# Kernel optimization log

Hardware: AMD Instinct MI355X
Metric: run time of the kernel (lower is better)

The kernel has to match this reference:

```python
import jax, jax.numpy as jnp
import numpy as np

D_MODEL = 1024
N_HEADS = 16
D_K = D_MODEL // N_HEADS
D_FF = 4096
B, S = 2, 2048
EPS = 1e-5
SCALE = 0.02


def setup_inputs() -> dict:
    key = jax.random.key(0)
    ks = jax.random.split(key, 8)
    return {
        "x": jax.random.normal(ks[0], (B, S, D_MODEL), dtype=jnp.float32),
        "ln1_w": jnp.ones((D_MODEL,), jnp.float32),
        "ln1_b": jnp.zeros((D_MODEL,), jnp.float32),
        "Wq": jax.random.normal(ks[1], (D_MODEL, D_MODEL), jnp.float32) * SCALE,
        "bq": jnp.zeros((D_MODEL,), jnp.float32),
        "Wk": jax.random.normal(ks[2], (D_MODEL, D_MODEL), jnp.float32) * SCALE,
        "bk": jnp.zeros((D_MODEL,), jnp.float32),
        "Wv": jax.random.normal(ks[3], (D_MODEL, D_MODEL), jnp.float32) * SCALE,
        "bv": jnp.zeros((D_MODEL,), jnp.float32),
        "Wo": jax.random.normal(ks[4], (D_MODEL, D_MODEL), jnp.float32) * SCALE,
        "bo": jnp.zeros((D_MODEL,), jnp.float32),
        "ln2_w": jnp.ones((D_MODEL,), jnp.float32),
        "ln2_b": jnp.zeros((D_MODEL,), jnp.float32),
        "W1": jax.random.normal(ks[5], (D_MODEL, D_FF), jnp.float32) * SCALE,
        "b1": jnp.zeros((D_FF,), jnp.float32),
        "W2": jax.random.normal(ks[6], (D_FF, D_MODEL), jnp.float32) * SCALE,
        "b2": jnp.zeros((D_MODEL,), jnp.float32),
    }


def _layernorm(x, w, b):
    mu = jnp.mean(x, axis=-1, keepdims=True)
    var = jnp.mean(jnp.square(x - mu), axis=-1, keepdims=True)
    return (x - mu) * jax.lax.rsqrt(var + EPS) * w + b


def reference(x, ln1_w, ln1_b, Wq, bq, Wk, bk, Wv, bv, Wo, bo,
              ln2_w, ln2_b, W1, b1, W2, b2):
    # Pre-norm multi-head self-attention (dropout = identity, eval mode)
    h = _layernorm(x, ln1_w, ln1_b)                      # [B,S,D]
    q = (h @ Wq + bq).reshape(B, S, N_HEADS, D_K)        # [B,S,H,Dk]
    k = (h @ Wk + bk).reshape(B, S, N_HEADS, D_K)
    v = (h @ Wv + bv).reshape(B, S, N_HEADS, D_K)
    scores = jnp.einsum('bqhd,bkhd->bhqk', q, k) / jnp.sqrt(jnp.float32(D_K))
    attn = jax.nn.softmax(scores, axis=-1)               # [B,H,S,S]
    ctx = jnp.einsum('bhqk,bkhd->bqhd', attn, v).reshape(B, S, D_MODEL)
    x = x + (ctx @ Wo + bo)
    # Pre-norm FFN
    h2 = _layernorm(x, ln2_w, ln2_b)
    ff = jax.nn.relu(h2 @ W1 + b1) @ W2 + b2
    return x + ff
```

## Files before the change

### kernel.cpp

```cpp
#include <hip/hip_runtime.h>
#include <hip/hip_bf16.h>
#include <cstdint>
#include <cstddef>

typedef unsigned short ushort_t;
typedef __bf16 bf16x8 __attribute__((ext_vector_type(8)));
typedef float f32x4 __attribute__((ext_vector_type(4)));
typedef float f32x16 __attribute__((ext_vector_type(16)));

#define D_MODEL 1024
#define D_FF 4096
#define BB 2
#define SS 2048
#define NH 16
#define MROWS (BB * SS)
#define KVBLK 64

__device__ __forceinline__ ushort_t f2bf(float f) {
  union { float f; unsigned u; } x; x.f = f;
  unsigned r = x.u + 0x7fffu + ((x.u >> 16) & 1u);
  return (ushort_t)(r >> 16);
}

__device__ __forceinline__ void gload_lds16(const void* g, void* l) {
  __builtin_amdgcn_global_load_lds((const __attribute__((address_space(1))) void*)g,
                                   (__attribute__((address_space(3))) void*)l, 16, 0, 0);
}

__device__ __forceinline__ bf16x8 pack4w(unsigned w0, unsigned w1, unsigned w2, unsigned w3) {
  union { unsigned u[4]; bf16x8 v; } t;
  t.u[0] = w0; t.u[1] = w1; t.u[2] = w2; t.u[3] = w3;
  return t.v;
}

__global__ __launch_bounds__(256) void ln_bf16_kernel(
    const float* __restrict__ x, const float* __restrict__ w,
    const float* __restrict__ b, ushort_t* __restrict__ out) {
  int row = blockIdx.x;
  int tid = threadIdx.x;
  int lane = tid & 63, wid = tid >> 6;
  const float4 v = ((const float4*)(x + (size_t)row * D_MODEL))[tid];
  float s = v.x + v.y + v.z + v.w;
  __shared__ float red[8];
  #pragma unroll
  for (int o = 32; o > 0; o >>= 1) s += __shfl_down(s, o);
  if (lane == 0) red[wid] = s;
  __syncthreads();
  float mu = (red[0] + red[1] + red[2] + red[3]) * (1.0f / D_MODEL);
  float d0 = v.x - mu, d1 = v.y - mu, d2 = v.z - mu, d3 = v.w - mu;
  float sq = d0 * d0 + d1 * d1 + d2 * d2 + d3 * d3;
  #pragma unroll
  for (int o = 32; o > 0; o >>= 1) sq += __shfl_down(sq, o);
  if (lane == 0) red[4 + wid] = sq;
  __syncthreads();
  float var = (red[4] + red[5] + red[6] + red[7]) * (1.0f / D_MODEL);
  float rstd = rsqrtf(var + 1e-5f);
  const float4 wv = ((const float4*)w)[tid];
  const float4 bv = ((const float4*)b)[tid];
  ushort4 o4;
  o4.x = f2bf(d0 * rstd * wv.x + bv.x);
  o4.y = f2bf(d1 * rstd * wv.y + bv.y);
  o4.z = f2bf(d2 * rstd * wv.z + bv.z);
  o4.w = f2bf(d3 * rstd * wv.w + bv.w);
  ((ushort4*)(out + (size_t)row * D_MODEL))[tid] = o4;
}

__global__ __launch_bounds__(256) void transpose_cast_kernel(
    const float* __restrict__ W, ushort_t* __restrict__ Wt, int K, int N) {
  __shared__ float tile[32][33];
  int bx = blockIdx.x * 32;
  int by = blockIdx.y * 32;
  int tx = threadIdx.x, ty = threadIdx.y;
  #pragma unroll
  for (int i = 0; i < 32; i += 8)
    tile[ty + i][tx] = W[(size_t)(by + ty + i) * N + bx + tx];
  __syncthreads();
  #pragma unroll
  for (int i = 0; i < 32; i += 8)
    Wt[(size_t)(bx + ty + i) * K + by + tx] = f2bf(tile[tx][ty + i]);
}

__global__ __launch_bounds__(256) void transpose_cast4_kernel(
    const float* __restrict__ Wq, const float* __restrict__ Wk,
    const float* __restrict__ Wv, const float* __restrict__ Wo,
    ushort_t* __restrict__ Dqkv, ushort_t* __restrict__ Do_) {
  __shared__ float tile[32][33];
  int z = blockIdx.z;
  const float* W = (z == 0) ? Wq : (z == 1) ? Wk : (z == 2) ? Wv : Wo;
  ushort_t* Wt = (z < 3) ? (Dqkv + (size_t)z * 1024 * 1024) : Do_;
  int bx = blockIdx.x * 32;
  int by = blockIdx.y * 32;
  int tx = threadIdx.x, ty = threadIdx.y;
  #pragma unroll
  for (int i = 0; i < 32; i += 8)
    tile[ty + i][tx] = W[(size_t)(by + ty + i) * 1024 + bx + tx];
  __syncthreads();
  #pragma unroll
  for (int i = 0; i < 32; i += 8)
    Wt[(size_t)(bx + ty + i) * 1024 + by + tx] = f2bf(tile[tx][ty + i]);
}

__global__ __launch_bounds__(256) void biaspack_kernel(
    const float* __restrict__ bq, const float* __restrict__ bk,
    const float* __restrict__ bv, float* __restrict__ out) {
  int i = blockIdx.x * 256 + threadIdx.x;
  float v = (i < 1024) ? bq[i] : (i < 2048) ? bk[i - 1024] : bv[i - 2048];
  out[i] = v;
}

__global__ __launch_bounds__(256) void vtrans_kernel(
    const ushort_t* __restrict__ qkv, ushort_t* __restrict__ Vt) {
  __shared__ __align__(16) ushort_t T[64 * 64];
  const int tid = threadIdx.x;
  const int bh = blockIdx.y, b = bh >> 4, h = bh & 15;
  const int kv0 = blockIdx.x * 64;
  const ushort_t* Vp = qkv + (size_t)b * SS * 3072 + 2048 + h * 64;
  #pragma unroll
  for (int i = 0; i < 2; i++) {
    int idx = tid * 2 + i;
    int key = idx >> 3, c = idx & 7;
    bf16x8 v = *(const bf16x8*)(Vp + (size_t)(kv0 + key) * 3072 + c * 8);
    *(bf16x8*)(T + key * 64 + ((c ^ (key & 7)) * 8)) = v;
  }
  __syncthreads();
  int d = tid >> 2, kb = tid & 3;
  ushort_t o[16];
  #pragma unroll
  for (int j = 0; j < 16; j++) {
    int key = kb * 16 + j;
    o[j] = T[key * 64 + (((d >> 3) ^ (key & 7)) * 8) + (d & 7)];
  }
  ushort_t* dst = Vt + (size_t)(bh * 64 + d) * SS + kv0 + kb * 16;
  *(bf16x8*)dst = *(bf16x8*)&o[0];
  *(bf16x8*)(dst + 8) = *(bf16x8*)&o[8];
}

template <int EPI>
__global__ __launch_bounds__(256, 3) void gemm128_kernel(
    const ushort_t* __restrict__ A, const ushort_t* __restrict__ Bt,
    const float* __restrict__ bias, const float* __restrict__ resid,
    void* __restrict__ Cout, int M, int N, int K, int NTn, int Ksplit, int MTN) {
  __shared__ __align__(16) ushort_t lds[3][2][4096];
  const int tid = threadIdx.x, lane = tid & 63, wid = tid >> 6;
  const int wm = wid >> 1, wn = wid & 1;
  const int rl = lane & 15, cg = lane >> 4;
  int nwg = gridDim.x;
  int q = nwg >> 3, rr = nwg & 7;
  int xcd = blockIdx.x & 7, idx = blockIdx.x >> 3;
  int wgid = (xcd < rr ? xcd * (q + 1) : rr * (q + 1) + (xcd - rr) * q) + idx;
  const int s = wgid / MTN;
  int rem = wgid - s * MTN;
  const int row0 = (rem / NTn) * 128, col0 = (rem - (rem / NTn) * NTn) * 128;
  const int k0 = s * Ksplit;
  const int NT = Ksplit / 32;

  int soff[2], ldso[2];
  #pragma unroll
  for (int i = 0; i < 2; i++) {
    int ci = wid * 128 + i * 64 + lane;
    int P = ci * 16;
    int L = P ^ (((P >> 7) & 7) << 4);
    int row = L >> 6, kc = (L >> 4) & 3;
    soff[i] = row * K + kc * 8;
    ldso[i] = (wid * 128 + i * 64) * 8;
  }

  f32x4 acc[4][4] = {};

  auto stage = [&](int t, int b) {
    int kk = k0 + t * 32;
    #pragma unroll
    for (int i = 0; i < 2; i++) {
      gload_lds16(A + (size_t)row0 * K + kk + soff[i], &lds[b][0][ldso[i]]);
      gload_lds16(Bt + (size_t)col0 * K + kk + soff[i], &lds[b][1][ldso[i]]);
    }
  };

  auto compute = [&](int b) {
    bf16x8 af[4], bfv[4];
    #pragma unroll
    for (int mi = 0; mi < 4; mi++) {
      int r = wm * 64 + mi * 16 + rl;
      int L = r * 64 + cg * 16;
      int P = L ^ (((L >> 7) & 7) << 4);
      af[mi] = *(const bf16x8*)&lds[b][0][P >> 1];
    }
    #pragma unroll
    for (int ni = 0; ni < 4; ni++) {
      int r = wn * 64 + ni * 16 + rl;
      int L = r * 64 + cg * 16;
      int P = L ^ (((L >> 7) & 7) << 4);
      bfv[ni] = *(const bf16x8*)&lds[b][1][P >> 1];
    }
    __builtin_amdgcn_s_setprio(1);
    #pragma unroll
    for (int mi = 0; mi < 4; mi++)
      #pragma unroll
      for (int ni = 0; ni < 4; ni++)
        acc[mi][ni] = __builtin_amdgcn_mfma_f32_16x16x32_bf16(af[mi], bfv[ni], acc[mi][ni], 0, 0, 0);
    __builtin_amdgcn_s_setprio(0);
  };

  stage(0, 0); stage(1, 1);
  int sb = 2, cb = 0;
  for (int t = 0; t < NT; ++t) {
    if (t < NT - 1) asm volatile("s_waitcnt vmcnt(4)" ::: "memory");
    else            asm volatile("s_waitcnt vmcnt(0)" ::: "memory");
    __builtin_amdgcn_s_barrier();
    __builtin_amdgcn_sched_barrier(0);
    if (t + 2 < NT) { stage(t + 2, sb); sb = (sb == 2) ? 0 : sb + 1; }
    compute(cb);
    cb = (cb == 2) ? 0 : cb + 1;
  }

  if (EPI == 2) {
    float* out = (float*)Cout;
    #pragma unroll
    for (int ni = 0; ni < 4; ni++) {
      int col = col0 + wn * 64 + ni * 16 + rl;
      float bv = bias[col];
      #pragma unroll
      for (int mi = 0; mi < 4; mi++) {
        int rowb = row0 + wm * 64 + mi * 16 + cg * 4;
        #pragma unroll
        for (int j = 0; j < 4; j++)
          out[(size_t)(rowb + j) * N + col] =
              acc[mi][ni][j] + bv + resid[(size_t)(rowb + j) * N + col];
      }
    }
  } else if (EPI == 3) {
    float* out = (float*)Cout + (size_t)s * M * N;
    #pragma unroll
    for (int ni = 0; ni < 4; ni++) {
      int col = col0 + wn * 64 + ni * 16 + rl;
      #pragma unroll
      for (int mi = 0; mi < 4; mi++) {
        int rowb = row0 + wm * 64 + mi * 16 + cg * 4;
        #pragma unroll
        for (int j = 0; j < 4; j++)
          out[(size_t)(rowb + j) * N + col] = acc[mi][ni][j];
      }
    }
  } else {
    ushort_t* out = (ushort_t*)Cout;
    #pragma unroll
    for (int ni = 0; ni < 4; ni++) {
      int col = col0 + wn * 64 + ni * 16 + rl;
      float bv = bias[col];
      float sc = (EPI == 0 && col < 1024) ? 0.18033688011f : 1.0f;
      #pragma unroll
      for (int mi = 0; mi < 4; mi++) {
        int rowb = row0 + wm * 64 + mi * 16 + cg * 4;
        #pragma unroll
        for (int j = 0; j < 4; j++) {
          float v = acc[mi][ni][j] + bv;
          if (EPI == 1) v = fmaxf(v, 0.0f);
          if (EPI == 0) v *= sc;
          out[(size_t)(rowb + j) * N + col] = f2bf(v);
        }
      }
    }
  }
}

__global__ __launch_bounds__(256) void reduce_kernel(
    const float* __restrict__ p, const float* __restrict__ bias,
    const float* __restrict__ resid, float* __restrict__ out,
    int S, size_t total4, size_t stride4) {
  const float4* p4 = (const float4*)p;
  const float4* r4 = (const float4*)resid;
  const float4* b4 = (const float4*)bias;
  float4* o4 = (float4*)out;
  for (size_t i = (size_t)blockIdx.x * 256 + threadIdx.x; i < total4;
       i += (size_t)gridDim.x * 256) {
    float4 a = r4[i];
    float4 bb = b4[i & 255];
    a.x += bb.x; a.y += bb.y; a.z += bb.z; a.w += bb.w;
    for (int s = 0; s < S; ++s) {
      float4 v = p4[(size_t)s * stride4 + i];
      a.x += v.x; a.y += v.y; a.z += v.z; a.w += v.w;
    }
    o4[i] = a;
  }
}

__global__ __launch_bounds__(256) void attn_kernel(
    const ushort_t* __restrict__ qkv, const ushort_t* __restrict__ Vt,
    ushort_t* __restrict__ ctx) {
  __shared__ __align__(16) ushort_t Kl[2][64 * 64];
  __shared__ __align__(16) ushort_t Vl[2][64 * 64];
  __shared__ float Lt[4][32];
  const int tid = threadIdx.x, lane = tid & 63, wid = tid >> 6;
  int bid = blockIdx.y * 16 + blockIdx.x;
  int w = (bid & 7) * 64 + (bid >> 3);
  const int bh = w >> 4, qt = w & 15;
  const int b = bh >> 4, h = bh & 15;
  const int q0w = qt * 128 + wid * 32;
  const int k31 = lane & 31, sg = lane >> 5, x7 = k31 & 7;
  const ushort_t* Qp = qkv + (size_t)b * SS * 3072 + h * 64;
  const ushort_t* Kp = Qp + 1024;
  const ushort_t* Vg = Vt + (size_t)bh * 64 * SS;

  bf16x8 qf[4];
  {
    const ushort_t* qb = Qp + (size_t)(q0w + k31) * 3072 + sg * 8;
    #pragma unroll
    for (int dsl = 0; dsl < 4; dsl++)
      qf[dsl] = *(const bf16x8*)(qb + dsl * 16);
  }
  float lsum = 0.f;
  f32x16 o0 = {}, o1 = {};

  const int NT = SS / KVBLK;

  int ksrc[2], vsrc[2];
  #pragma unroll
  for (int i = 0; i < 2; i++) {
    int idx = wid * 128 + i * 64 + lane;
    int R = idx >> 3, c = idx & 7;
    ksrc[i] = R * 3072 + ((c ^ (R & 7)) * 8);
    vsrc[i] = R * SS + ((c ^ (R & 7)) * 8);
  }
  const int ldsb = wid * 1024;

  auto stageKV = [&](int buf, int t) {
    size_t kvK = (size_t)t * KVBLK * 3072;
    int kvV = t * KVBLK;
    gload_lds16(Kp + kvK + ksrc[0], &Kl[buf][ldsb]);
    gload_lds16(Kp + kvK + ksrc[1], &Kl[buf][ldsb + 512]);
    gload_lds16(Vg + kvV + vsrc[0], &Vl[buf][ldsb]);
    gload_lds16(Vg + kvV + vsrc[1], &Vl[buf][ldsb + 512]);
  };

  auto softmax_half = [&](const f32x16& s, bf16x8& paE, bf16x8& paO) {
    float pv[16];
    #pragma unroll
    for (int r = 0; r < 16; r++) pv[r] = __builtin_amdgcn_exp2f(s[r]);
    #pragma unroll
    for (int r = 0; r < 16; r++) lsum += pv[r];
    unsigned W[4][2];
    #pragma unroll
    for (int qd = 0; qd < 4; qd++) {
      asm("v_cvt_pk_bf16_f32 %0, %1, %2" : "=v"(W[qd][0]) : "v"(pv[4 * qd]), "v"(pv[4 * qd + 1]));
      asm("v_cvt_pk_bf16_f32 %0, %1, %2" : "=v"(W[qd][1]) : "v"(pv[4 * qd + 2]), "v"(pv[4 * qd + 3]));
    }
    unsigned a0 = W[1][0], b0 = W[0][0], a1 = W[1][1], b1 = W[0][1];
    asm("v_permlane32_swap_b32 %0, %1" : "+v"(a0), "+v"(b0));
    asm("v_permlane32_swap_b32 %0, %1" : "+v"(a1), "+v"(b1));
    paE = pack4w(b0, b1, a0, a1);
    unsigned a2 = W[3][0], b2 = W[2][0], a3 = W[3][1], b3 = W[2][1];
    asm("v_permlane32_swap_b32 %0, %1" : "+v"(a2), "+v"(b2));
    asm("v_permlane32_swap_b32 %0, %1" : "+v"(a3), "+v"(b3));
    paO = pack4w(b2, b3, a2, a3);
  };

  auto body = [&](int t, int cb) {
    __syncthreads();
    if (t + 1 < NT) stageKV(cb ^ 1, t + 1);

    f32x16 s0 = {}, s1 = {};
    #pragma unroll
    for (int dsl = 0; dsl < 4; dsl++) {
      int ch = ((dsl * 2 + sg) ^ x7) * 8;
      bf16x8 kf0 = *(const bf16x8*)(&Kl[cb][k31 * 64 + ch]);
      bf16x8 kf1 = *(const bf16x8*)(&Kl[cb][(32 + k31) * 64 + ch]);
      s0 = __builtin_amdgcn_mfma_f32_32x32x16_bf16(kf0, qf[dsl], s0, 0, 0, 0);
      s1 = __builtin_amdgcn_mfma_f32_32x32x16_bf16(kf1, qf[dsl], s1, 0, 0, 0);
    }
    bf16x8 pa[4];
    softmax_half(s0, pa[0], pa[1]);
    softmax_half(s1, pa[2], pa[3]);
    #pragma unroll
    for (int ks = 0; ks < 4; ks++) {
      int ch = ((2 * ks + sg) ^ x7) * 8;
      bf16x8 vf0 = *(const bf16x8*)(&Vl[cb][k31 * 64 + ch]);
      bf16x8 vf1 = *(const bf16x8*)(&Vl[cb][(32 + k31) * 64 + ch]);
      o0 = __builtin_amdgcn_mfma_f32_32x32x16_bf16(pa[ks], vf0, o0, 0, 0, 0);
      o1 = __builtin_amdgcn_mfma_f32_32x32x16_bf16(pa[ks], vf1, o1, 0, 0, 0);
    }
  };

  stageKV(0, 0);
  for (int t = 0; t < NT; t += 2) {
    body(t, 0);
    body(t + 1, 1);
  }

  float ltot = lsum + __shfl_xor(lsum, 32);
  if (lane < 32) Lt[wid][lane] = ltot;
  asm volatile("s_waitcnt lgkmcnt(0)" ::: "memory");
  __builtin_amdgcn_sched_barrier(0);

  const int colb = h * 64 + k31;
  #pragma unroll
  for (int r = 0; r < 16; r++) {
    int qp = (r & 3) + 8 * (r >> 2) + 4 * sg;
    float rlq = 1.0f / Lt[wid][qp];
    size_t row = (size_t)(b * SS + q0w + qp);
    ctx[row * D_MODEL + colb] = f2bf(o0[r] * rlq);
    ctx[row * D_MODEL + colb + 32] = f2bf(o1[r] * rlq);
  }
}

extern "C" void kernel_launch(void* const* d_in, const int* in_sizes, int n_in,
                              void* d_out, int out_size, void* d_ws, size_t ws_size,
                              hipStream_t stream) {
  const float* x    = (const float*)d_in[0];
  const float* ln1w = (const float*)d_in[1];
  const float* ln1b = (const float*)d_in[2];
  const float* Wq   = (const float*)d_in[3];
  const float* bq   = (const float*)d_in[4];
  const float* Wk   = (const float*)d_in[5];
  const float* bk   = (const float*)d_in[6];
  const float* Wv   = (const float*)d_in[7];
  const float* bv   = (const float*)d_in[8];
  const float* Wo   = (const float*)d_in[9];
  const float* bo   = (const float*)d_in[10];
  const float* ln2w = (const float*)d_in[11];
  const float* ln2b = (const float*)d_in[12];
  const float* W1   = (const float*)d_in[13];
  const float* b1   = (const float*)d_in[14];
  const float* W2   = (const float*)d_in[15];
  const float* b2   = (const float*)d_in[16];

  char* ws = (char*)d_ws;
  size_t off = 0;
  auto alloc = [&](size_t bytes) {
    void* p = ws + off;
    off += (bytes + 255) & ~(size_t)255;
    return p;
  };
  ushort_t* Wt_qkv = (ushort_t*)alloc((size_t)3072 * 1024 * 2);
  ushort_t* Wt_o   = (ushort_t*)alloc((size_t)1024 * 1024 * 2);
  ushort_t* Wt_1   = (ushort_t*)alloc((size_t)4096 * 1024 * 2);
  ushort_t* Wt_2   = (ushort_t*)alloc((size_t)1024 * 4096 * 2);
  float*    bqkv   = (float*)alloc((size_t)3072 * 4);
  ushort_t* qkvb   = (ushort_t*)alloc((size_t)MROWS * 3072 * 2);
  ushort_t* ctxb   = (ushort_t*)alloc((size_t)MROWS * 1024 * 2);
  ushort_t* hbuf   = (ushort_t*)alloc((size_t)MROWS * 1024 * 2);
  float*    x2     = (float*)alloc((size_t)MROWS * 1024 * 4);
  ushort_t* Vtb    = (ushort_t*)alloc((size_t)BB * NH * 64 * SS * 2);
  ushort_t* ff1    = qkvb;
  float*    outp   = (float*)d_out;

  const size_t partial1 = (size_t)MROWS * 1024 * 4;
  int S = (ws_size - off >= 2 * partial1 + 256) ? 2 : 1;
  float* pbuf = (S == 2) ? (float*)alloc(2 * partial1) : nullptr;

  dim3 tb(32, 8);
  transpose_cast4_kernel<<<dim3(32, 32, 4), tb, 0, stream>>>(Wq, Wk, Wv, Wo, Wt_qkv, Wt_o);
  transpose_cast_kernel<<<dim3(128, 32), tb, 0, stream>>>(W1, Wt_1, 1024, 4096);
  transpose_cast_kernel<<<dim3(32, 128), tb, 0, stream>>>(W2, Wt_2, 4096, 1024);
  biaspack_kernel<<<12, 256, 0, stream>>>(bq, bk, bv, bqkv);

  ln_bf16_kernel<<<MROWS, 256, 0, stream>>>(x, ln1w, ln1b, hbuf);
  gemm128_kernel<0><<<dim3(24 * 32), 256, 0, stream>>>(
      hbuf, Wt_qkv, bqkv, nullptr, qkvb, MROWS, 3072, 1024, 24, 1024, 24 * 32);
  vtrans_kernel<<<dim3(SS / 64, BB * NH), 256, 0, stream>>>(qkvb, Vtb);
  attn_kernel<<<dim3(SS / 128, BB * NH), 256, 0, stream>>>(qkvb, Vtb, ctxb);
  gemm128_kernel<2><<<dim3(8 * 32), 256, 0, stream>>>(
      ctxb, Wt_o, bo, x, x2, MROWS, 1024, 1024, 8, 1024, 8 * 32);
  ln_bf16_kernel<<<MROWS, 256, 0, stream>>>(x2, ln2w, ln2b, hbuf);
  gemm128_kernel<1><<<dim3(32 * 32), 256, 0, stream>>>(
      hbuf, Wt_1, b1, nullptr, ff1, MROWS, D_FF, 1024, 32, 1024, 32 * 32);
  if (S == 2) {
    gemm128_kernel<3><<<dim3(8 * 32 * 2), 256, 0, stream>>>(
        ff1, Wt_2, nullptr, nullptr, pbuf, MROWS, 1024, 4096, 8, 2048, 8 * 32);
    reduce_kernel<<<2048, 256, 0, stream>>>(pbuf, b2, x2, outp, 2,
        (size_t)MROWS * 1024 / 4, (size_t)MROWS * 1024 / 4);
  } else {
    gemm128_kernel<2><<<dim3(8 * 32), 256, 0, stream>>>(
        ff1, Wt_2, b2, x2, outp, MROWS, 1024, 4096, 8, 4096, 8 * 32);
  }
}
```

Baseline: 234.9 us.

## Use 128x256 wide-tile GEMM kernel for QKV and FFN1 projections

Adds a new GEMM kernel with 128x256 output tiles (each wave computes 64x128 with 4x8 MFMA accumulators) and triple-buffered LDS, and uses it for the QKV and first FFN projections. Wider tiles raise arithmetic intensity and cut redundant A-tile loads, at the cost of more registers, lower occupancy (launch bounds 2), and fewer workgroups (384 and 512), which may underfill the 256 CUs. The old bf16 epilogue path in gemm128 is removed because it is no longer used.

```diff
diff --git a/kernel.cpp b/kernel.cpp
--- a/kernel.cpp
+++ b/kernel.cpp
@@ -133,6 +133,110 @@
   ushort_t* dst = Vt + (size_t)(bh * 64 + d) * SS + kv0 + kb * 16;
   *(bf16x8*)dst = *(bf16x8*)&o[0];
   *(bf16x8*)(dst + 8) = *(bf16x8*)&o[8];
+}
+
+template <int EPI>
+__global__ __launch_bounds__(256, 2) void gemm256w_kernel(
+    const ushort_t* __restrict__ A, const ushort_t* __restrict__ Bt,
+    const float* __restrict__ bias, void* __restrict__ Cout,
+    int M, int N, int K, int NTn) {
+  __shared__ __align__(16) ushort_t ldsA[3][4096];
+  __shared__ __align__(16) ushort_t ldsB[3][8192];
+  const int tid = threadIdx.x, lane = tid & 63, wid = tid >> 6;
+  const int wm = wid >> 1, wn = wid & 1;
+  const int rl = lane & 15, cg = lane >> 4;
+  int nwg = gridDim.x;
+  int q = nwg >> 3, rr = nwg & 7;
+  int xcd = blockIdx.x & 7, idx = blockIdx.x >> 3;
+  int wgid = (xcd < rr ? xcd * (q + 1) : rr * (q + 1) + (xcd - rr) * q) + idx;
+  const int row0 = (wgid / NTn) * 128, col0 = (wgid - (wgid / NTn) * NTn) * 256;
+  const int NT = K / 32;
+
+  int soffA[2], ldsoA[2], soffB[4], ldsoB[4];
+  #pragma unroll
+  for (int i = 0; i < 2; i++) {
+    int ci = wid * 128 + i * 64 + lane;
+    int P = ci * 16;
+    int L = P ^ (((P >> 7) & 7) << 4);
+    soffA[i] = (L >> 6) * K + ((L >> 4) & 3) * 8;
+    ldsoA[i] = (wid * 128 + i * 64) * 8;
+  }
+  #pragma unroll
+  for (int i = 0; i < 4; i++) {
+    int ci = wid * 256 + i * 64 + lane;
+    int P = ci * 16;
+    int L = P ^ (((P >> 7) & 7) << 4);
+    soffB[i] = (L >> 6) * K + ((L >> 4) & 3) * 8;
+    ldsoB[i] = (wid * 256 + i * 64) * 8;
+  }
+
+  f32x4 acc[4][8] = {};
+
+  auto stage = [&](int t, int b) {
+    int kk = t * 32;
+    #pragma unroll
+    for (int i = 0; i < 2; i++)
+      gload_lds16(A + (size_t)row0 * K + kk + soffA[i], &ldsA[b][ldsoA[i]]);
+    #pragma unroll
+    for (int i = 0; i < 4; i++)
+      gload_lds16(Bt + (size_t)col0 * K + kk + soffB[i], &ldsB[b][ldsoB[i]]);
+  };
+
+  auto compute = [&](int b) {
+    bf16x8 af[4], bfv[8];
+    #pragma unroll
+    for (int mi = 0; mi < 4; mi++) {
+      int r = wm * 64 + mi * 16 + rl;
+      int L = r * 64 + cg * 16;
+      int P = L ^ (((L >> 7) & 7) << 4);
+      af[mi] = *(const bf16x8*)&ldsA[b][P >> 1];
+    }
+    #pragma unroll
+    for (int ni = 0; ni < 8; ni++) {
+      int r = wn * 128 + ni * 16 + rl;
+      int L = r * 64 + cg * 16;
+      int P = L ^ (((L >> 7) & 7) << 4);
+      bfv[ni] = *(const bf16x8*)&ldsB[b][P >> 1];
+    }
+    __builtin_amdgcn_s_setprio(1);
+    #pragma unroll
+    for (int mi = 0; mi < 4; mi++)
+      #pragma unroll
+      for (int ni = 0; ni < 8; ni++)
+        acc[mi][ni] = __builtin_amdgcn_mfma_f32_16x16x32_bf16(af[mi], bfv[ni], acc[mi][ni], 0, 0, 0);
+    __builtin_amdgcn_s_setprio(0);
+  };
+
+  stage(0, 0); stage(1, 1);
+  int sb = 2, cb = 0;
+  for (int t = 0; t < NT; ++t) {
+    if (t < NT - 1) asm volatile("s_waitcnt vmcnt(6)" ::: "memory");
+    else            asm volatile("s_waitcnt vmcnt(0)" ::: "memory");
+    __builtin_amdgcn_s_barrier();
+    __builtin_amdgcn_sched_barrier(0);
+    if (t + 2 < NT) { stage(t + 2, sb); sb = (sb == 2) ? 0 : sb + 1; }
+    compute(cb);
+    cb = (cb == 2) ? 0 : cb + 1;
+  }
+
+  ushort_t* out = (ushort_t*)Cout;
+  #pragma unroll
+  for (int ni = 0; ni < 8; ni++) {
+    int col = col0 + wn * 128 + ni * 16 + rl;
+    float bv = bias[col];
+    float sc = (EPI == 0 && col < 1024) ? 0.18033688011f : 1.0f;
+    #pragma unroll
+    for (int mi = 0; mi < 4; mi++) {
+      int rowb = row0 + wm * 64 + mi * 16 + cg * 4;
+      #pragma unroll
+      for (int j = 0; j < 4; j++) {
+        float v = acc[mi][ni][j] + bv;
+        if (EPI == 1) v = fmaxf(v, 0.0f);
+        if (EPI == 0) v *= sc;
+        out[(size_t)(rowb + j) * N + col] = f2bf(v);
+      }
+    }
+  }
 }
 
 template <int EPI>
@@ -228,7 +332,7 @@
               acc[mi][ni][j] + bv + resid[(size_t)(rowb + j) * N + col];
       }
     }
-  } else if (EPI == 3) {
+  } else {
     float* out = (float*)Cout + (size_t)s * M * N;
     #pragma unroll
     for (int ni = 0; ni < 4; ni++) {
@@ -239,25 +343,6 @@
         #pragma unroll
         for (int j = 0; j < 4; j++)
           out[(size_t)(rowb + j) * N + col] = acc[mi][ni][j];
-      }
-    }
-  } else {
-    ushort_t* out = (ushort_t*)Cout;
-    #pragma unroll
-    for (int ni = 0; ni < 4; ni++) {
-      int col = col0 + wn * 64 + ni * 16 + rl;
-      float bv = bias[col];
-      float sc = (EPI == 0 && col < 1024) ? 0.18033688011f : 1.0f;
-      #pragma unroll
-      for (int mi = 0; mi < 4; mi++) {
-        int rowb = row0 + wm * 64 + mi * 16 + cg * 4;
-        #pragma unroll
-        for (int j = 0; j < 4; j++) {
-          float v = acc[mi][ni][j] + bv;
-          if (EPI == 1) v = fmaxf(v, 0.0f);
-          if (EPI == 0) v *= sc;
-          out[(size_t)(rowb + j) * N + col] = f2bf(v);
-        }
       }
     }
   }
@@ -454,15 +539,15 @@
   biaspack_kernel<<<12, 256, 0, stream>>>(bq, bk, bv, bqkv);
 
   ln_bf16_kernel<<<MROWS, 256, 0, stream>>>(x, ln1w, ln1b, hbuf);
-  gemm128_kernel<0><<<dim3(24 * 32), 256, 0, stream>>>(
-      hbuf, Wt_qkv, bqkv, nullptr, qkvb, MROWS, 3072, 1024, 24, 1024, 24 * 32);
+  gemm256w_kernel<0><<<dim3(32 * 12), 256, 0, stream>>>(
+      hbuf, Wt_qkv, bqkv, qkvb, MROWS, 3072, 1024, 12);
   vtrans_kernel<<<dim3(SS / 64, BB * NH), 256, 0, stream>>>(qkvb, Vtb);
   attn_kernel<<<dim3(SS / 128, BB * NH), 256, 0, stream>>>(qkvb, Vtb, ctxb);
   gemm128_kernel<2><<<dim3(8 * 32), 256, 0, stream>>>(
       ctxb, Wt_o, bo, x, x2, MROWS, 1024, 1024, 8, 1024, 8 * 32);
   ln_bf16_kernel<<<MROWS, 256, 0, stream>>>(x2, ln2w, ln2b, hbuf);
-  gemm128_kernel<1><<<dim3(32 * 32), 256, 0, stream>>>(
-      hbuf, Wt_1, b1, nullptr, ff1, MROWS, D_FF, 1024, 32, 1024, 32 * 32);
+  gemm256w_kernel<1><<<dim3(32 * 16), 256, 0, stream>>>(
+      hbuf, Wt_1, b1, ff1, MROWS, D_FF, 1024, 16);
   if (S == 2) {
     gemm128_kernel<3><<<dim3(8 * 32 * 2), 256, 0, stream>>>(
         ff1, Wt_2, nullptr, nullptr, pbuf, MROWS, 1024, 4096, 8, 2048, 8 * 32);
```

Result: no change. 232.2 us (-1.2%).
